# Optimization experiments

Measured on AMD Instinct MI355X. Metric: run time of the kernel, lower is better.

Reference implementation:

```python
import jax, jax.numpy as jnp
import numpy as np
import math

N_HEADS = 16
SINK_STRENGTH = 0.1


def setup_inputs() -> dict:
    key = jax.random.key(0)
    ks = jax.random.split(key, 16)
    B, S, D = 2, 2048, 1024
    sd = 1.0 / math.sqrt(D)
    return {
        "query": jax.random.normal(ks[0], (B, S, D), jnp.float32),
        "key_": jax.random.normal(ks[1], (B, S, D), jnp.float32),
        "value": jax.random.normal(ks[2], (B, S, D), jnp.float32),
        "positions": jax.random.uniform(ks[3], (B, S), jnp.float32),
        "attention_mask": jnp.ones((B, S), jnp.int32),
        "Wq": jax.random.normal(ks[4], (D, D), jnp.float32) * sd,
        "bq": jnp.zeros((D,), jnp.float32),
        "Wk": jax.random.normal(ks[5], (D, D), jnp.float32) * sd,
        "bk": jnp.zeros((D,), jnp.float32),
        "Wv": jax.random.normal(ks[6], (D, D), jnp.float32) * sd,
        "bv": jnp.zeros((D,), jnp.float32),
        "Wo": jax.random.normal(ks[7], (D, D), jnp.float32) * sd,
        "bo": jnp.zeros((D,), jnp.float32),
    }


def reference(query, key_, value, positions, attention_mask, Wq, bq, Wk, bk, Wv, bv, Wo, bo):
    B, S, D = query.shape
    H = N_HEADS
    hd = D // H
    scale = 1.0 / math.sqrt(hd)

    def split_heads(x):  # [B,S,D] -> [B,H,S,hd]
        return x.reshape(B, S, H, hd).transpose(0, 2, 1, 3)

    q = split_heads(query @ Wq.T + bq)
    k = split_heads(key_ @ Wk.T + bk)
    v = split_heads(value @ Wv.T + bv)

    scores = jnp.einsum("bhqd,bhkd->bhqk", q, k) * scale  # [B,H,S,S]

    # sink index: argmin of positions over valid (mask!=0) tokens, per batch
    masked_pos = jnp.where(attention_mask == 0, jnp.inf, positions)
    sink_indices = jnp.argmin(masked_pos, axis=-1)  # [B]

    # per-batch sink bias: add sink_strength to every score column at sink index
    sink_onehot = jax.nn.one_hot(sink_indices, S, dtype=scores.dtype)  # [B,S]
    scores = scores + SINK_STRENGTH * sink_onehot[:, None, None, :]

    # key-side padding mask
    scores = jnp.where(attention_mask[:, None, None, :] == 0, -1e9, scores)

    probs = jax.nn.softmax(scores, axis=-1)
    out = jnp.einsum("bhqk,bhkd->bhqd", probs, v)  # [B,H,S,hd]
    out = out.transpose(0, 2, 1, 3).reshape(B, S, D)
    return out @ Wo.T + bo, sink_indices
```

## Files before the change

kernel.cpp:

```cpp
#include <hip/hip_runtime.h>
#include <hip/hip_bf16.h>
#include <math.h>

constexpr int B  = 2;
constexpr int S  = 2048;
constexpr int D  = 1024;
constexpr int H  = 16;
constexpr int HD = 64;
constexpr float SINK_STRENGTH = 0.1f;
constexpr float LOG2E  = 1.4426950408889634f;
constexpr float SCALE2 = 0.125f * LOG2E;
constexpr float THR2   = 8.0f * LOG2E;

typedef short v4s __attribute__((ext_vector_type(4)));
typedef short v8s __attribute__((ext_vector_type(8)));
typedef float v4f __attribute__((ext_vector_type(4)));

__device__ inline float exp2_fast(float x) {
  return __builtin_amdgcn_exp2f(x);
}

__device__ inline v4f mfma_16x16x32_bf16(v8s a, v8s b, v4f c) {
  return __builtin_amdgcn_mfma_f32_16x16x32_bf16(a, b, c, 0, 0, 0);
}

__device__ inline v4f mfma_16x16x16_bf16(v4s a, v4s b, v4f c) {
#if defined(__has_builtin)
#if __has_builtin(__builtin_amdgcn_mfma_f32_16x16x16bf16_1k)
  return __builtin_amdgcn_mfma_f32_16x16x16bf16_1k(a, b, c, 0, 0, 0);
#define MFMA16_DONE 1
#endif
#endif
#ifndef MFMA16_DONE
  v4f d;
  asm volatile("v_mfma_f32_16x16x16_bf16 %0, %1, %2, %3"
               : "=v"(d) : "v"(a), "v"(b), "v"(c));
  return d;
#endif
}

__device__ inline unsigned short f2bf(float f) {
  __hip_bfloat16 h = __float2bfloat16(f);
  return *reinterpret_cast<unsigned short*>(&h);
}

__device__ inline ushort4 pack4(float4 f) {
  return make_ushort4(f2bf(f.x), f2bf(f.y), f2bf(f.z), f2bf(f.w));
}

__device__ inline void gld16(const void* g, void* l) {
  __builtin_amdgcn_global_load_lds(
      (const __attribute__((address_space(1))) void*)g,
      (__attribute__((address_space(3))) void*)l, 16, 0, 0);
}

__device__ inline void stage8(const unsigned char* gbase, size_t gstride,
                              unsigned char* ldsbase, int rb, int lane) {
  const int r = rb + (lane >> 3);
  const int c = (lane & 7) * 16;
  const unsigned char* g = gbase + (size_t)r * gstride + (c ^ ((r & 7) << 4));
  gld16(g, ldsbase + rb * 128);
}

__device__ inline unsigned swz(int row, int bytecol) {
  return (unsigned)(row * 128 + (bytecol ^ ((row & 7) << 4)));
}

struct CvtArgs {
  const float* src[7];
  unsigned short* dst[7];
  int n[7];
};

__global__ __launch_bounds__(256) void convert_kernel(CvtArgs a) {
  const int t = blockIdx.y;
  const float* s = a.src[t];
  unsigned short* d = a.dst[t];
  const int n = a.n[t];
  for (int i = (blockIdx.x * 256 + threadIdx.x) * 8; i < n;
       i += gridDim.x * 256 * 8) {
    float4 f0 = *reinterpret_cast<const float4*>(s + i);
    float4 f1 = *reinterpret_cast<const float4*>(s + i + 4);
    *reinterpret_cast<ushort4*>(d + i)     = pack4(f0);
    *reinterpret_cast<ushort4*>(d + i + 4) = pack4(f1);
  }
}

__global__ void sink_kernel(const float* __restrict__ pos,
                            const int* __restrict__ mask,
                            float* __restrict__ sbias_g,
                            float* __restrict__ out_tail, int tail_elems) {
  const int b = blockIdx.x;
  __shared__ float sval[256];
  __shared__ int   sidx[256];
  float best = INFINITY;
  int   bidx = 0x7fffffff;
  for (int i = threadIdx.x; i < S; i += 256) {
    float v = (mask[b * S + i] == 0) ? INFINITY : pos[b * S + i];
    if (v < best || (v == best && i < bidx)) { best = v; bidx = i; }
  }
  sval[threadIdx.x] = best;
  sidx[threadIdx.x] = bidx;
  __syncthreads();
  for (int off = 128; off > 0; off >>= 1) {
    if ((int)threadIdx.x < off) {
      float v  = sval[threadIdx.x + off];
      int   ix = sidx[threadIdx.x + off];
      if (v < sval[threadIdx.x] ||
          (v == sval[threadIdx.x] && ix < sidx[threadIdx.x])) {
        sval[threadIdx.x] = v;
        sidx[threadIdx.x] = ix;
      }
    }
    __syncthreads();
  }
  const int sb = sidx[0];
  if (threadIdx.x == 0 && b < tail_elems) out_tail[b] = (float)sb;
  for (int i = threadIdx.x; i < S; i += 256)
    sbias_g[b * S + i] =
        (mask[b * S + i] ? ((i == sb) ? SINK_STRENGTH : 0.f) : -1e9f) * LOG2E;
}

struct QKVArgs {
  const unsigned short* x[3];
  const unsigned short* w[3];
  const float* bias[3];
  unsigned short* y[3];
};

__global__ __launch_bounds__(256) void gemm_qkv(QKVArgs args) {
  __shared__ __align__(16) unsigned char lds[2 * 32768];
  int id = blockIdx.x;
  id = (id & 7) * 96 + (id >> 3);
  const int z = id >> 8, rem = id & 255;
  const int m0 = (rem >> 3) * 128, n0 = (rem & 7) * 128;

  const int tid = threadIdx.x, lane = tid & 63, w = tid >> 6;
  const int wr = w >> 1, wc = w & 1, lr = lane & 15, g = lane >> 4;
  const unsigned short* X  = args.x[z];
  const unsigned short* Wb = args.w[z];
  const unsigned char* xg = (const unsigned char*)(X + (size_t)m0 * D);
  const unsigned char* wg = (const unsigned char*)(Wb + (size_t)n0 * D);
  const size_t stride = (size_t)D * 2;

  auto stage = [&](int buf, int k0) {
    unsigned char* Xs = lds + buf * 32768;
    unsigned char* Ws = Xs + 16384;
    const unsigned char* xk = xg + (size_t)k0 * 2;
    const unsigned char* wk = wg + (size_t)k0 * 2;
#pragma unroll
    for (int u = 0; u < 4; ++u) stage8(xk, stride, Xs, w * 32 + u * 8, lane);
#pragma unroll
    for (int u = 0; u < 4; ++u) stage8(wk, stride, Ws, w * 32 + u * 8, lane);
  };

  stage(0, 0);
  v4f acc[4][4] = {};
  const int ksteps = D / 64;
  int cur = 0;
  for (int s = 0; s < ksteps; ++s) {
    __syncthreads();
    if (s + 1 < ksteps) stage(cur ^ 1, (s + 1) * 64);
    const unsigned char* Xs = lds + cur * 32768;
    const unsigned char* Ws = Xs + 16384;
    const int sw = (lr & 7) << 4;
#pragma unroll
    for (int ks = 0; ks < 2; ++ks) {
      v8s a[4], bb[4];
#pragma unroll
      for (int mf = 0; mf < 4; ++mf)
        a[mf] = *reinterpret_cast<const v8s*>(
            Xs + (wr * 64 + mf * 16 + lr) * 128 + ((ks * 64 + g * 16) ^ sw));
#pragma unroll
      for (int nf = 0; nf < 4; ++nf)
        bb[nf] = *reinterpret_cast<const v8s*>(
            Ws + (wc * 64 + nf * 16 + lr) * 128 + ((ks * 64 + g * 16) ^ sw));
#pragma unroll
      for (int mf = 0; mf < 4; ++mf)
#pragma unroll
        for (int nf = 0; nf < 4; ++nf)
          acc[mf][nf] = mfma_16x16x32_bf16(a[mf], bb[nf], acc[mf][nf]);
    }
    cur ^= 1;
  }

  const float* bias = args.bias[z];
  unsigned short* Y = args.y[z];
  if (z < 2) {
#pragma unroll
    for (int nf = 0; nf < 4; ++nf) {
      const int n = n0 + wc * 64 + nf * 16 + lr;
      const float bs = bias[n];
#pragma unroll
      for (int mf = 0; mf < 4; ++mf)
#pragma unroll
        for (int r = 0; r < 4; ++r)
          Y[(size_t)(m0 + wr * 64 + mf * 16 + g * 4 + r) * D + n] =
              f2bf(acc[mf][nf][r] + bs);
    }
  } else {
#pragma unroll
    for (int nf = 0; nf < 4; ++nf) {
      const int n = n0 + wc * 64 + nf * 16 + lr;
      const int hh = n >> 6, dd = n & 63;
      const float bs = bias[n];
#pragma unroll
      for (int mf = 0; mf < 4; ++mf) {
        const int m = m0 + wr * 64 + mf * 16 + g * 4;
        const int bb2 = m >> 11, ss = m & 2047;
        float4 f = make_float4(acc[mf][nf][0] + bs, acc[mf][nf][1] + bs,
                               acc[mf][nf][2] + bs, acc[mf][nf][3] + bs);
        *reinterpret_cast<ushort4*>(
            &Y[(((size_t)bb2 * H + hh) * HD + dd) * S + ss]) = pack4(f);
      }
    }
  }
}

__global__ __launch_bounds__(256) void gemm_o(
    const unsigned short* __restrict__ X, const unsigned short* __restrict__ Wb,
    const float* __restrict__ bias, float* __restrict__ Y) {
  __shared__ __align__(16) unsigned char lds[2 * 24576];
  const int tid = threadIdx.x, lane = tid & 63, w = tid >> 6;
  const int wr = w >> 1, wc = w & 1, lr = lane & 15, g = lane >> 4;
  const int m0 = blockIdx.y * 128, n0 = blockIdx.x * 64;
  const unsigned char* xg = (const unsigned char*)(X + (size_t)m0 * D);
  const unsigned char* wg = (const unsigned char*)(Wb + (size_t)n0 * D);
  const size_t stride = (size_t)D * 2;

  auto stage = [&](int buf, int k0) {
    unsigned char* Xs = lds + buf * 24576;
    unsigned char* Ws = Xs + 16384;
    const unsigned char* xk = xg + (size_t)k0 * 2;
    const unsigned char* wk = wg + (size_t)k0 * 2;
#pragma unroll
    for (int u = 0; u < 4; ++u) stage8(xk, stride, Xs, w * 32 + u * 8, lane);
#pragma unroll
    for (int u = 0; u < 2; ++u) stage8(wk, stride, Ws, w * 16 + u * 8, lane);
  };

  stage(0, 0);
  v4f acc[4][2] = {};
  const int ksteps = D / 64;
  int cur = 0;
  for (int s = 0; s < ksteps; ++s) {
    __syncthreads();
    if (s + 1 < ksteps) stage(cur ^ 1, (s + 1) * 64);
    const unsigned char* Xs = lds + cur * 24576;
    const unsigned char* Ws = Xs + 16384;
    const int sw = (lr & 7) << 4;
#pragma unroll
    for (int ks = 0; ks < 2; ++ks) {
      v8s a[4], bf2[2];
#pragma unroll
      for (int mf = 0; mf < 4; ++mf)
        a[mf] = *reinterpret_cast<const v8s*>(
            Xs + (wr * 64 + mf * 16 + lr) * 128 + ((ks * 64 + g * 16) ^ sw));
#pragma unroll
      for (int nf = 0; nf < 2; ++nf)
        bf2[nf] = *reinterpret_cast<const v8s*>(
            Ws + (wc * 32 + nf * 16 + lr) * 128 + ((ks * 64 + g * 16) ^ sw));
#pragma unroll
      for (int mf = 0; mf < 4; ++mf)
#pragma unroll
        for (int nf = 0; nf < 2; ++nf)
          acc[mf][nf] = mfma_16x16x32_bf16(a[mf], bf2[nf], acc[mf][nf]);
    }
    cur ^= 1;
  }
#pragma unroll
  for (int nf = 0; nf < 2; ++nf) {
    const int n = n0 + wc * 32 + nf * 16 + lr;
    const float bs = bias[n];
#pragma unroll
    for (int mf = 0; mf < 4; ++mf)
#pragma unroll
      for (int r = 0; r < 4; ++r)
        Y[(size_t)(m0 + wr * 64 + mf * 16 + g * 4 + r) * D + n] =
            acc[mf][nf][r] + bs;
  }
}

__global__ __launch_bounds__(256) void attn_kernel(
    const unsigned short* __restrict__ qg, const unsigned short* __restrict__ kg,
    const unsigned short* __restrict__ vt, const float* __restrict__ sbias_g,
    unsigned short* __restrict__ og) {
  __shared__ __align__(16) unsigned char smem[8192 + 2 * 16384];
  int id = blockIdx.x;
  id = (id & 7) * 128 + (id >> 3);
  const int q0 = (id & 31) * 64, hb = id >> 5;
  const int h = hb & 15, b = hb >> 4;

  const int tid = threadIdx.x, lane = tid & 63, wv = tid >> 6;
  const int lr = lane & 15, g = lane >> 4;

  const unsigned char* qgb =
      (const unsigned char*)(qg + ((size_t)b * S + q0) * D + h * HD);
  const unsigned char* kgb0 =
      (const unsigned char*)(kg + (size_t)b * S * D + h * HD);
  const unsigned char* vtb =
      (const unsigned char*)(vt + ((size_t)b * H + h) * HD * S);

  stage8(qgb, D * 2, smem, wv * 16, lane);
  stage8(qgb, D * 2, smem, wv * 16 + 8, lane);
  {
    unsigned char* Ks = smem + 8192;
    unsigned char* Vs = Ks + 8192;
    stage8(kgb0, D * 2, Ks, wv * 16, lane);
    stage8(kgb0, D * 2, Ks, wv * 16 + 8, lane);
    stage8(vtb, S * 2, Vs, wv * 16, lane);
    stage8(vtb, S * 2, Vs, wv * 16 + 8, lane);
  }
  __syncthreads();
  v8s qf[2];
  qf[0] = *reinterpret_cast<const v8s*>(smem + swz(wv * 16 + lr, g * 16));
  qf[1] = *reinterpret_cast<const v8s*>(smem + swz(wv * 16 + lr, 64 + g * 16));

  float m_i = -INFINITY, l_i = 0.f;
  v4f acc[4] = {};
  int cur = 0;

  for (int kv0 = 0; kv0 < S; kv0 += 64) {
    const unsigned char* Ks = smem + 8192 + cur * 16384;
    const unsigned char* Vs = Ks + 8192;

    float4 b4[4];
#pragma unroll
    for (int t = 0; t < 4; ++t)
      b4[t] = *reinterpret_cast<const float4*>(
          &sbias_g[b * S + kv0 + t * 16 + g * 4]);

    if (kv0 + 64 < S) {
      unsigned char* Kn = smem + 8192 + (cur ^ 1) * 16384;
      unsigned char* Vn = Kn + 8192;
      const unsigned char* kgb = kgb0 + (size_t)(kv0 + 64) * (D * 2);
      const unsigned char* vgb = vtb + (size_t)(kv0 + 64) * 2;
      stage8(kgb, D * 2, Kn, wv * 16, lane);
      stage8(kgb, D * 2, Kn, wv * 16 + 8, lane);
      stage8(vgb, S * 2, Vn, wv * 16, lane);
      stage8(vgb, S * 2, Vn, wv * 16 + 8, lane);
    }

    v4f st[4] = {};
    __builtin_amdgcn_s_setprio(1);
#pragma unroll
    for (int t = 0; t < 4; ++t) {
#pragma unroll
      for (int ks = 0; ks < 2; ++ks) {
        v8s aK = *reinterpret_cast<const v8s*>(
            Ks + swz(t * 16 + lr, ks * 64 + g * 16));
        st[t] = mfma_16x16x32_bf16(aK, qf[ks], st[t]);
      }
    }
    __builtin_amdgcn_s_setprio(0);

    float s[4][4];
    float mx = -INFINITY;
#pragma unroll
    for (int t = 0; t < 4; ++t) {
      const float bb[4] = {b4[t].x, b4[t].y, b4[t].z, b4[t].w};
#pragma unroll
      for (int r = 0; r < 4; ++r) s[t][r] = fmaf(st[t][r], SCALE2, bb[r]);
      mx = fmaxf(mx, fmaxf(fmaxf(s[t][0], s[t][1]), fmaxf(s[t][2], s[t][3])));
    }
    mx = fmaxf(mx, __shfl_xor(mx, 16, 64));
    mx = fmaxf(mx, __shfl_xor(mx, 32, 64));

    if (__any(mx > m_i + THR2)) {
      const float mn   = fmaxf(m_i, mx);
      const float corr = exp2_fast(m_i - mn);
      l_i *= corr;
#pragma unroll
      for (int c = 0; c < 4; ++c) acc[c] = acc[c] * corr;
      m_i = mn;
    }

    float rs = 0.f;
    v4s pb[4];
#pragma unroll
    for (int t = 0; t < 4; ++t) {
#pragma unroll
      for (int r = 0; r < 4; ++r) {
        float pv = exp2_fast(s[t][r] - m_i);
        rs += pv;
        pb[t][r] = (short)f2bf(pv);
      }
    }
    rs += __shfl_xor(rs, 16, 64);
    rs += __shfl_xor(rs, 32, 64);
    l_i += rs;

    __builtin_amdgcn_s_setprio(1);
#pragma unroll
    for (int t = 0; t < 4; ++t) {
#pragma unroll
      for (int c = 0; c < 4; ++c) {
        v4s aV = *reinterpret_cast<const v4s*>(
            Vs + swz(c * 16 + lr, t * 32 + g * 8));
        acc[c] = mfma_16x16x16_bf16(aV, pb[t], acc[c]);
      }
    }
    __builtin_amdgcn_s_setprio(0);

    __syncthreads();
    cur ^= 1;
  }

  const float inv = 1.0f / l_i;
  unsigned short* orow = og + ((size_t)b * S + q0 + wv * 16 + lr) * D + h * HD;
#pragma unroll
  for (int c = 0; c < 4; ++c) {
    float4 f = make_float4(acc[c][0] * inv, acc[c][1] * inv, acc[c][2] * inv,
                           acc[c][3] * inv);
    *reinterpret_cast<ushort4*>(orow + c * 16 + g * 4) = pack4(f);
  }
}

extern "C" void kernel_launch(void* const* d_in, const int* in_sizes, int n_in,
                              void* d_out, int out_size, void* d_ws,
                              size_t ws_size, hipStream_t stream) {
  const float* query = (const float*)d_in[0];
  const float* key_  = (const float*)d_in[1];
  const float* value = (const float*)d_in[2];
  const float* pos   = (const float*)d_in[3];
  const int*   amask = (const int*)d_in[4];
  const float* Wq = (const float*)d_in[5];
  const float* bq = (const float*)d_in[6];
  const float* Wk = (const float*)d_in[7];
  const float* bk = (const float*)d_in[8];
  const float* Wv = (const float*)d_in[9];
  const float* bv = (const float*)d_in[10];
  const float* Wo = (const float*)d_in[11];
  const float* bo = (const float*)d_in[12];
  float* out = (float*)d_out;

  constexpr size_t NBSD = (size_t)B * S * D;
  constexpr size_t NDD  = (size_t)D * D;
  unsigned short* qx  = (unsigned short*)d_ws;
  unsigned short* kx  = qx + NBSD;
  unsigned short* vx  = kx + NBSD;
  unsigned short* wqb = vx + NBSD;
  unsigned short* wkb = wqb + NDD;
  unsigned short* wvb = wkb + NDD;
  unsigned short* wob = wvb + NDD;
  unsigned short* qb  = wob + NDD;
  unsigned short* kb  = qb + NBSD;
  unsigned short* vt  = kb + NBSD;
  float* sbias_g = (float*)(vt + NBSD);
  unsigned short* ab = qx;

  CvtArgs ca;
  ca.src[0] = query; ca.dst[0] = qx;  ca.n[0] = (int)NBSD;
  ca.src[1] = key_;  ca.dst[1] = kx;  ca.n[1] = (int)NBSD;
  ca.src[2] = value; ca.dst[2] = vx;  ca.n[2] = (int)NBSD;
  ca.src[3] = Wq;    ca.dst[3] = wqb; ca.n[3] = (int)NDD;
  ca.src[4] = Wk;    ca.dst[4] = wkb; ca.n[4] = (int)NDD;
  ca.src[5] = Wv;    ca.dst[5] = wvb; ca.n[5] = (int)NDD;
  ca.src[6] = Wo;    ca.dst[6] = wob; ca.n[6] = (int)NDD;
  convert_kernel<<<dim3(2048, 7), 256, 0, stream>>>(ca);

  const int tail_elems = out_size - (int)NBSD;
  sink_kernel<<<B, 256, 0, stream>>>(pos, amask, sbias_g, out + NBSD,
                                     tail_elems);

  QKVArgs qa;
  qa.x[0] = qx; qa.w[0] = wqb; qa.bias[0] = bq; qa.y[0] = qb;
  qa.x[1] = kx; qa.w[1] = wkb; qa.bias[1] = bk; qa.y[1] = kb;
  qa.x[2] = vx; qa.w[2] = wvb; qa.bias[2] = bv; qa.y[2] = vt;
  gemm_qkv<<<768, 256, 0, stream>>>(qa);

  attn_kernel<<<1024, 256, 0, stream>>>(qb, kb, vt, sbias_g, ab);

  gemm_o<<<dim3(D / 64, (B * S) / 128), 256, 0, stream>>>(ab, wob, bo, out);
}
```

Baseline: 260.4 us.

## Double query rows per attention block, compute row sums via MFMA, widen output GEMM tile

The attention kernel now handles 128 queries per block as two 64-row strips that share each staged K/V tile, halving K/V global traffic and LDS staging per query. The softmax denominator is accumulated with an MFMA against a ones vector instead of shuffle reductions, so it uses bf16-rounded probabilities. The output projection GEMM moves from 128x64 to 128x128 tiles with a swizzled 1D grid for better reuse. In exchange, registers and LDS per block go up and the grids shrink to 512 and 256 blocks, which may lower occupancy on a 256-CU device.

```diff
diff --git a/kernel.cpp b/kernel.cpp
--- a/kernel.cpp
+++ b/kernel.cpp
@@ -220,57 +220,61 @@
 __global__ __launch_bounds__(256) void gemm_o(
     const unsigned short* __restrict__ X, const unsigned short* __restrict__ Wb,
     const float* __restrict__ bias, float* __restrict__ Y) {
-  __shared__ __align__(16) unsigned char lds[2 * 24576];
+  __shared__ __align__(16) unsigned char lds[2 * 32768];
+  int id = blockIdx.x;
+  id = (id & 7) * 32 + (id >> 3);
+  const int m0 = (id >> 3) * 128, n0 = (id & 7) * 128;
+
   const int tid = threadIdx.x, lane = tid & 63, w = tid >> 6;
   const int wr = w >> 1, wc = w & 1, lr = lane & 15, g = lane >> 4;
-  const int m0 = blockIdx.y * 128, n0 = blockIdx.x * 64;
   const unsigned char* xg = (const unsigned char*)(X + (size_t)m0 * D);
   const unsigned char* wg = (const unsigned char*)(Wb + (size_t)n0 * D);
   const size_t stride = (size_t)D * 2;
 
   auto stage = [&](int buf, int k0) {
-    unsigned char* Xs = lds + buf * 24576;
+    unsigned char* Xs = lds + buf * 32768;
     unsigned char* Ws = Xs + 16384;
     const unsigned char* xk = xg + (size_t)k0 * 2;
     const unsigned char* wk = wg + (size_t)k0 * 2;
 #pragma unroll
     for (int u = 0; u < 4; ++u) stage8(xk, stride, Xs, w * 32 + u * 8, lane);
 #pragma unroll
-    for (int u = 0; u < 2; ++u) stage8(wk, stride, Ws, w * 16 + u * 8, lane);
+    for (int u = 0; u < 4; ++u) stage8(wk, stride, Ws, w * 32 + u * 8, lane);
   };
 
   stage(0, 0);
-  v4f acc[4][2] = {};
+  v4f acc[4][4] = {};
   const int ksteps = D / 64;
   int cur = 0;
   for (int s = 0; s < ksteps; ++s) {
     __syncthreads();
     if (s + 1 < ksteps) stage(cur ^ 1, (s + 1) * 64);
-    const unsigned char* Xs = lds + cur * 24576;
+    const unsigned char* Xs = lds + cur * 32768;
     const unsigned char* Ws = Xs + 16384;
     const int sw = (lr & 7) << 4;
 #pragma unroll
     for (int ks = 0; ks < 2; ++ks) {
-      v8s a[4], bf2[2];
+      v8s a[4], bb[4];
 #pragma unroll
       for (int mf = 0; mf < 4; ++mf)
         a[mf] = *reinterpret_cast<const v8s*>(
             Xs + (wr * 64 + mf * 16 + lr) * 128 + ((ks * 64 + g * 16) ^ sw));
 #pragma unroll
-      for (int nf = 0; nf < 2; ++nf)
-        bf2[nf] = *reinterpret_cast<const v8s*>(
-            Ws + (wc * 32 + nf * 16 + lr) * 128 + ((ks * 64 + g * 16) ^ sw));
+      for (int nf = 0; nf < 4; ++nf)
+        bb[nf] = *reinterpret_cast<const v8s*>(
+            Ws + (wc * 64 + nf * 16 + lr) * 128 + ((ks * 64 + g * 16) ^ sw));
 #pragma unroll
       for (int mf = 0; mf < 4; ++mf)
 #pragma unroll
-        for (int nf = 0; nf < 2; ++nf)
-          acc[mf][nf] = mfma_16x16x32_bf16(a[mf], bf2[nf], acc[mf][nf]);
+        for (int nf = 0; nf < 4; ++nf)
+          acc[mf][nf] = mfma_16x16x32_bf16(a[mf], bb[nf], acc[mf][nf]);
     }
     cur ^= 1;
   }
-#pragma unroll
-  for (int nf = 0; nf < 2; ++nf) {
-    const int n = n0 + wc * 32 + nf * 16 + lr;
+
+#pragma unroll
+  for (int nf = 0; nf < 4; ++nf) {
+    const int n = n0 + wc * 64 + nf * 16 + lr;
     const float bs = bias[n];
 #pragma unroll
     for (int mf = 0; mf < 4; ++mf)
@@ -285,10 +289,10 @@
     const unsigned short* __restrict__ qg, const unsigned short* __restrict__ kg,
     const unsigned short* __restrict__ vt, const float* __restrict__ sbias_g,
     unsigned short* __restrict__ og) {
-  __shared__ __align__(16) unsigned char smem[8192 + 2 * 16384];
+  __shared__ __align__(16) unsigned char smem[16384 + 2 * 16384];
   int id = blockIdx.x;
-  id = (id & 7) * 128 + (id >> 3);
-  const int q0 = (id & 31) * 64, hb = id >> 5;
+  id = (id & 7) * 64 + (id >> 3);
+  const int q0 = (id & 15) * 128, hb = id >> 4;
   const int h = hb & 15, b = hb >> 4;
 
   const int tid = threadIdx.x, lane = tid & 63, wv = tid >> 6;
@@ -301,10 +305,10 @@
   const unsigned char* vtb =
       (const unsigned char*)(vt + ((size_t)b * H + h) * HD * S);
 
-  stage8(qgb, D * 2, smem, wv * 16, lane);
-  stage8(qgb, D * 2, smem, wv * 16 + 8, lane);
+#pragma unroll
+  for (int u = 0; u < 4; ++u) stage8(qgb, D * 2, smem, wv * 32 + u * 8, lane);
   {
-    unsigned char* Ks = smem + 8192;
+    unsigned char* Ks = smem + 16384;
     unsigned char* Vs = Ks + 8192;
     stage8(kgb0, D * 2, Ks, wv * 16, lane);
     stage8(kgb0, D * 2, Ks, wv * 16 + 8, lane);
@@ -312,26 +316,63 @@
     stage8(vtb, S * 2, Vs, wv * 16 + 8, lane);
   }
   __syncthreads();
-  v8s qf[2];
-  qf[0] = *reinterpret_cast<const v8s*>(smem + swz(wv * 16 + lr, g * 16));
-  qf[1] = *reinterpret_cast<const v8s*>(smem + swz(wv * 16 + lr, 64 + g * 16));
-
-  float m_i = -INFINITY, l_i = 0.f;
-  v4f acc[4] = {};
+  v8s qf0[2], qf1[2];
+#pragma unroll
+  for (int ks = 0; ks < 2; ++ks) {
+    qf0[ks] = *reinterpret_cast<const v8s*>(
+        smem + swz(wv * 16 + lr, ks * 64 + g * 16));
+    qf1[ks] = *reinterpret_cast<const v8s*>(
+        smem + swz(64 + wv * 16 + lr, ks * 64 + g * 16));
+  }
+
+  const v4s vones = {(short)0x3F80, (short)0x3F80, (short)0x3F80,
+                     (short)0x3F80};
+  float m0_ = -INFINITY, m1_ = -INFINITY;
+  v4f acc0[4] = {}, acc1[4] = {};
+  v4f accl0 = {}, accl1 = {};
+  float4 b4[4];
   int cur = 0;
 
+  auto softmax_strip = [&](v4f (&st)[4], float& m_, v4f (&acc)[4], v4f& accl,
+                           v4s (&pb)[4]) {
+    float s[4][4];
+    float mx = -INFINITY;
+#pragma unroll
+    for (int t = 0; t < 4; ++t) {
+      const float bbv[4] = {b4[t].x, b4[t].y, b4[t].z, b4[t].w};
+#pragma unroll
+      for (int r = 0; r < 4; ++r) s[t][r] = fmaf(st[t][r], SCALE2, bbv[r]);
+      mx = fmaxf(fmaxf(mx, fmaxf(s[t][0], s[t][1])),
+                 fmaxf(s[t][2], s[t][3]));
+    }
+    mx = fmaxf(mx, __shfl_xor(mx, 16, 64));
+    mx = fmaxf(mx, __shfl_xor(mx, 32, 64));
+    if (__any(mx > m_ + THR2)) {
+      const float mn   = fmaxf(m_, mx);
+      const float corr = exp2_fast(m_ - mn);
+#pragma unroll
+      for (int c = 0; c < 4; ++c) acc[c] = acc[c] * corr;
+      accl = accl * corr;
+      m_ = mn;
+    }
+#pragma unroll
+    for (int t = 0; t < 4; ++t)
+#pragma unroll
+      for (int r = 0; r < 4; ++r)
+        pb[t][r] = (short)f2bf(exp2_fast(s[t][r] - m_));
+  };
+
   for (int kv0 = 0; kv0 < S; kv0 += 64) {
-    const unsigned char* Ks = smem + 8192 + cur * 16384;
+    const unsigned char* Ks = smem + 16384 + cur * 16384;
     const unsigned char* Vs = Ks + 8192;
 
-    float4 b4[4];
 #pragma unroll
     for (int t = 0; t < 4; ++t)
       b4[t] = *reinterpret_cast<const float4*>(
           &sbias_g[b * S + kv0 + t * 16 + g * 4]);
 
     if (kv0 + 64 < S) {
-      unsigned char* Kn = smem + 8192 + (cur ^ 1) * 16384;
+      unsigned char* Kn = smem + 16384 + (cur ^ 1) * 16384;
       unsigned char* Vn = Kn + 8192;
       const unsigned char* kgb = kgb0 + (size_t)(kv0 + 64) * (D * 2);
       const unsigned char* vgb = vtb + (size_t)(kv0 + 64) * 2;
@@ -341,7 +382,7 @@
       stage8(vgb, S * 2, Vn, wv * 16 + 8, lane);
     }
 
-    v4f st[4] = {};
+    v4f st0[4] = {}, st1[4] = {};
     __builtin_amdgcn_s_setprio(1);
 #pragma unroll
     for (int t = 0; t < 4; ++t) {
@@ -349,55 +390,27 @@
       for (int ks = 0; ks < 2; ++ks) {
         v8s aK = *reinterpret_cast<const v8s*>(
             Ks + swz(t * 16 + lr, ks * 64 + g * 16));
-        st[t] = mfma_16x16x32_bf16(aK, qf[ks], st[t]);
+        st0[t] = mfma_16x16x32_bf16(aK, qf0[ks], st0[t]);
+        st1[t] = mfma_16x16x32_bf16(aK, qf1[ks], st1[t]);
       }
     }
     __builtin_amdgcn_s_setprio(0);
 
-    float s[4][4];
-    float mx = -INFINITY;
+    v4s pb0[4], pb1[4];
+    softmax_strip(st0, m0_, acc0, accl0, pb0);
+    softmax_strip(st1, m1_, acc1, accl1, pb1);
+
+    __builtin_amdgcn_s_setprio(1);
 #pragma unroll
     for (int t = 0; t < 4; ++t) {
-      const float bb[4] = {b4[t].x, b4[t].y, b4[t].z, b4[t].w};
-#pragma unroll
-      for (int r = 0; r < 4; ++r) s[t][r] = fmaf(st[t][r], SCALE2, bb[r]);
-      mx = fmaxf(mx, fmaxf(fmaxf(s[t][0], s[t][1]), fmaxf(s[t][2], s[t][3])));
-    }
-    mx = fmaxf(mx, __shfl_xor(mx, 16, 64));
-    mx = fmaxf(mx, __shfl_xor(mx, 32, 64));
-
-    if (__any(mx > m_i + THR2)) {
-      const float mn   = fmaxf(m_i, mx);
-      const float corr = exp2_fast(m_i - mn);
-      l_i *= corr;
-#pragma unroll
-      for (int c = 0; c < 4; ++c) acc[c] = acc[c] * corr;
-      m_i = mn;
-    }
-
-    float rs = 0.f;
-    v4s pb[4];
-#pragma unroll
-    for (int t = 0; t < 4; ++t) {
-#pragma unroll
-      for (int r = 0; r < 4; ++r) {
-        float pv = exp2_fast(s[t][r] - m_i);
-        rs += pv;
-        pb[t][r] = (short)f2bf(pv);
-      }
-    }
-    rs += __shfl_xor(rs, 16, 64);
-    rs += __shfl_xor(rs, 32, 64);
-    l_i += rs;
-
-    __builtin_amdgcn_s_setprio(1);
-#pragma unroll
-    for (int t = 0; t < 4; ++t) {
+      accl0 = mfma_16x16x16_bf16(vones, pb0[t], accl0);
+      accl1 = mfma_16x16x16_bf16(vones, pb1[t], accl1);
 #pragma unroll
       for (int c = 0; c < 4; ++c) {
         v4s aV = *reinterpret_cast<const v4s*>(
             Vs + swz(c * 16 + lr, t * 32 + g * 8));
-        acc[c] = mfma_16x16x16_bf16(aV, pb[t], acc[c]);
+        acc0[c] = mfma_16x16x16_bf16(aV, pb0[t], acc0[c]);
+        acc1[c] = mfma_16x16x16_bf16(aV, pb1[t], acc1[c]);
       }
     }
     __builtin_amdgcn_s_setprio(0);
@@ -406,13 +419,20 @@
     cur ^= 1;
   }
 
-  const float inv = 1.0f / l_i;
-  unsigned short* orow = og + ((size_t)b * S + q0 + wv * 16 + lr) * D + h * HD;
+  const float inv0 = 1.0f / accl0[0];
+  const float inv1 = 1.0f / accl1[0];
+  unsigned short* o0 =
+      og + ((size_t)b * S + q0 + wv * 16 + lr) * D + h * HD;
+  unsigned short* o1 =
+      og + ((size_t)b * S + q0 + 64 + wv * 16 + lr) * D + h * HD;
 #pragma unroll
   for (int c = 0; c < 4; ++c) {
-    float4 f = make_float4(acc[c][0] * inv, acc[c][1] * inv, acc[c][2] * inv,
-                           acc[c][3] * inv);
-    *reinterpret_cast<ushort4*>(orow + c * 16 + g * 4) = pack4(f);
+    float4 f0 = make_float4(acc0[c][0] * inv0, acc0[c][1] * inv0,
+                            acc0[c][2] * inv0, acc0[c][3] * inv0);
+    float4 f1 = make_float4(acc1[c][0] * inv1, acc1[c][1] * inv1,
+                            acc1[c][2] * inv1, acc1[c][3] * inv1);
+    *reinterpret_cast<ushort4*>(o0 + c * 16 + g * 4) = pack4(f0);
+    *reinterpret_cast<ushort4*>(o1 + c * 16 + g * 4) = pack4(f1);
   }
 }
 
@@ -469,7 +489,7 @@
   qa.x[2] = vx; qa.w[2] = wvb; qa.bias[2] = bv; qa.y[2] = vt;
   gemm_qkv<<<768, 256, 0, stream>>>(qa);
 
-  attn_kernel<<<1024, 256, 0, stream>>>(qb, kb, vt, sbias_g, ab);
-
-  gemm_o<<<dim3(D / 64, (B * S) / 128), 256, 0, stream>>>(ab, wob, bo, out);
-}
+  attn_kernel<<<512, 256, 0, stream>>>(qb, kb, vt, sbias_g, ab);
+
+  gemm_o<<<256, 256, 0, stream>>>(ab, wob, bo, out);
+}
```

After: 254.9 us. 2.1% less time.
